# Performance work log

Measured on AMD Instinct MI355X. Metric: run time of the kernel, lower is better.

The kernel has to match this reference:

```python
import math
import jax, jax.numpy as jnp
import numpy as np

B, N, DIM = 2, 4096, 768
H, DK, DV = 8, 64, 64


def setup_inputs() -> dict:
    key = jax.random.key(0)
    ks = jax.random.split(key, 6)
    s = 0.02
    return {
        "x": jax.random.normal(ks[0], (B, N, DIM), dtype=jnp.float32),
        "Wq": jax.random.normal(ks[1], (DIM, H * DK), dtype=jnp.float32) * s,
        "Wk": jax.random.normal(ks[2], (DIM, H * DK), dtype=jnp.float32) * s,
        "Wv": jax.random.normal(ks[3], (DIM, H * DV), dtype=jnp.float32) * s,
        "Wo": jax.random.normal(ks[4], (H * DV, DIM), dtype=jnp.float32) * s,
        "bo": jax.random.normal(ks[5], (DIM,), dtype=jnp.float32) * s,
    }


def reference(x, Wq, Wk, Wv, Wo, bo):
    b, n, _ = x.shape
    # project and split heads: [B, H, N, d]
    q = (x @ Wq).reshape(b, n, H, DK).transpose(0, 2, 1, 3)
    k = (x @ Wk).reshape(b, n, H, DK).transpose(0, 2, 1, 3)
    v = (x @ Wv).reshape(b, n, H, DV).transpose(0, 2, 1, 3)
    scale = 1.0 / math.sqrt(DK)
    scores = jnp.einsum("bhnd,bhmd->bhnm", q, k) * scale  # [B,H,N,N]
    attn = jax.nn.softmax(scores, axis=-1)
    out = jnp.einsum("bhnm,bhmd->bhnd", attn, v)  # [B,H,N,DV]
    out = out.transpose(0, 2, 1, 3).reshape(b, n, H * DV)
    return out @ Wo + bo
```

## Files before the change

kernel.cpp:

```cpp
#include <hip/hip_runtime.h>
#include <hip/hip_bf16.h>

#define B_   2
#define N_   4096
#define DIM_ 768
#define H_   8
#define MROWS_ 8192

typedef __bf16 bf16x8 __attribute__((ext_vector_type(8)));
typedef __bf16 bf16x4 __attribute__((ext_vector_type(4)));
typedef float  f32x4  __attribute__((ext_vector_type(4)));

static __device__ __forceinline__ f32x4 mfma16(bf16x8 a, bf16x8 b, f32x4 c) {
    return __builtin_amdgcn_mfma_f32_16x16x32_bf16(a, b, c, 0, 0, 0);
}

#define GLDS16(g, l) \
    __builtin_amdgcn_global_load_lds((const __attribute__((address_space(1))) void*)(g), \
                                     (__attribute__((address_space(3))) void*)(l), 16, 0, 0)

__global__ void cvt_x_kernel(const float* __restrict__ x, __bf16* __restrict__ xb, int n4) {
    int i = blockIdx.x * blockDim.x + threadIdx.x;
    if (i >= n4) return;
    float4 f = reinterpret_cast<const float4*>(x)[i];
    bf16x4 o;
    o[0] = (__bf16)f.x; o[1] = (__bf16)f.y; o[2] = (__bf16)f.z; o[3] = (__bf16)f.w;
    reinterpret_cast<bf16x4*>(xb)[i] = o;
}

__global__ __launch_bounds__(256) void transpose_w_kernel(const float* __restrict__ Wq,
                                                          const float* __restrict__ Wk,
                                                          const float* __restrict__ Wv,
                                                          const float* __restrict__ Wo,
                                                          __bf16* __restrict__ wt,
                                                          __bf16* __restrict__ wot) {
    __shared__ float tile[64][65];
    const int bix = blockIdx.x;
    const float* src;
    int src_ld, rbase, cbase, dst_ld, drow, dcol;
    __bf16* dst;
    if (bix < 288) {
        int m = bix / 96, t = bix - m * 96;
        int tr = t >> 3, tc = t & 7;
        src = (m == 0) ? Wq : ((m == 1) ? Wk : Wv);
        src_ld = 512; rbase = tr * 64; cbase = tc * 64;
        dst = wt; dst_ld = 768; drow = m * 512 + tc * 64; dcol = tr * 64;
    } else {
        int t = bix - 288;
        int tr = t / 12, tc = t - tr * 12;
        src = Wo; src_ld = 768; rbase = tr * 64; cbase = tc * 64;
        dst = wot; dst_ld = 512; drow = tc * 64; dcol = tr * 64;
    }
#pragma unroll
    for (int kk = 0; kk < 4; ++kk) {
        int idx = threadIdx.x + kk * 256;
        int r = idx >> 4, c = (idx & 15) << 2;
        float4 f = *reinterpret_cast<const float4*>(&src[(size_t)(rbase + r) * src_ld + cbase + c]);
        tile[r][c] = f.x; tile[r][c + 1] = f.y; tile[r][c + 2] = f.z; tile[r][c + 3] = f.w;
    }
    __syncthreads();
#pragma unroll
    for (int kk = 0; kk < 4; ++kk) {
        int idx = threadIdx.x + kk * 256;
        int r = idx >> 4, c = (idx & 15) << 2;
        bf16x4 ov;
        ov[0] = (__bf16)tile[c][r];     ov[1] = (__bf16)tile[c + 1][r];
        ov[2] = (__bf16)tile[c + 2][r]; ov[3] = (__bf16)tile[c + 3][r];
        *reinterpret_cast<bf16x4*>(&dst[(size_t)(drow + r) * dst_ld + dcol + c]) = ov;
    }
}

template<int KSTEPS>
__device__ __forceinline__ void gemm_tile_main(const __bf16* __restrict__ A, const int lda,
                                               const int arow0,
                                               const __bf16* __restrict__ Bt, const int ldb,
                                               const int bcol0,
                                               __bf16* __restrict__ abuf,
                                               __bf16* __restrict__ bbuf,
                                               f32x4 (&acc)[4][4]) {
    const int lane = threadIdx.x & 63, wave = threadIdx.x >> 6;
    const int lr = lane & 15, lg = lane >> 4;
    const int wr = wave >> 1, wc = wave & 1;

    const int cid0 = wave * 128 + lane;
    const int cid1 = cid0 + 64;
    const __bf16* sA0 = A  + (size_t)(arow0 + (cid0 >> 2)) * lda + (cid0 & 3) * 8;
    const __bf16* sA1 = A  + (size_t)(arow0 + (cid1 >> 2)) * lda + (cid1 & 3) * 8;
    const __bf16* sB0 = Bt + (size_t)(bcol0 + (cid0 >> 2)) * ldb + (cid0 & 3) * 8;
    const __bf16* sB1 = Bt + (size_t)(bcol0 + (cid1 >> 2)) * ldb + (cid1 & 3) * 8;

    auto stage = [&](int buf, int ks) {
        __bf16* da = abuf + buf * 4096 + wave * 1024;
        __bf16* db = bbuf + buf * 4096 + wave * 1024;
        GLDS16(sA0 + ks * 32, da);
        GLDS16(sA1 + ks * 32, da + 512);
        GLDS16(sB0 + ks * 32, db);
        GLDS16(sB1 + ks * 32, db + 512);
    };

    stage(0, 0);
    asm volatile("s_waitcnt vmcnt(0)" ::: "memory");
    __syncthreads();

    const int ar_off = (wr * 64 + lr) * 32 + lg * 8;
    const int br_off = (wc * 64 + lr) * 32 + lg * 8;

    int buf = 0;
    for (int ks = 0; ks < KSTEPS; ++ks) {
        if (ks + 1 < KSTEPS) stage(buf ^ 1, ks + 1);
        const __bf16* ab = abuf + buf * 4096 + ar_off;
        const __bf16* bb = bbuf + buf * 4096 + br_off;
        bf16x8 af[4], bfr[4];
#pragma unroll
        for (int m = 0; m < 4; ++m) af[m] = *reinterpret_cast<const bf16x8*>(ab + m * 512);
#pragma unroll
        for (int n = 0; n < 4; ++n) bfr[n] = *reinterpret_cast<const bf16x8*>(bb + n * 512);
#pragma unroll
        for (int m = 0; m < 4; ++m)
#pragma unroll
            for (int n = 0; n < 4; ++n)
                acc[m][n] = mfma16(af[m], bfr[n], acc[m][n]);
        asm volatile("s_waitcnt vmcnt(0)" ::: "memory");
        __syncthreads();
        buf ^= 1;
    }
}

__global__ __launch_bounds__(256) void qkv_gemm_kernel(const __bf16* __restrict__ xb,
                                                       const __bf16* __restrict__ wt,
                                                       __bf16* __restrict__ q,
                                                       __bf16* __restrict__ k,
                                                       __bf16* __restrict__ vt) {
    __shared__ __align__(16) __bf16 abuf[2 * 4096];
    __shared__ __align__(16) __bf16 bbuf[2 * 4096];

    const int bid = blockIdx.x;
    const int vb = (bid & 7) * 96 + (bid >> 3);
    const int by = vb % 12, bx = vb / 12;

    f32x4 acc[4][4] = {};
    gemm_tile_main<24>(xb, 768, bx * 128, wt, 768, by * 128, abuf, bbuf, acc);

    const int lane = threadIdx.x & 63, wave = threadIdx.x >> 6;
    const int lr = lane & 15, lg = lane >> 4;
    const int wr = wave >> 1, wc = wave & 1;
    const int bi = (bx * 128) >> 12;
    const int nbase = (bx * 128) & 4095;

    const float QSCALE = 0.125f * 1.44269504089f;

#pragma unroll
    for (int n = 0; n < 4; ++n) {
        const int col0 = by * 128 + wc * 64 + n * 16;
        const int mtx = col0 >> 9;
        const int h   = (col0 >> 6) & 7;
        const int d0  = (col0 & 63) + lr;
        const size_t hb = (size_t)(bi * 8 + h);
#pragma unroll
        for (int m = 0; m < 4; ++m) {
            const int nn = nbase + wr * 64 + m * 16 + lg * 4;
            if (mtx == 0) {
#pragma unroll
                for (int r = 0; r < 4; ++r)
                    q[(hb * 4096 + nn + r) * 64 + d0] = (__bf16)(acc[m][n][r] * QSCALE);
            } else if (mtx == 1) {
#pragma unroll
                for (int r = 0; r < 4; ++r)
                    k[(hb * 4096 + nn + r) * 64 + d0] = (__bf16)acc[m][n][r];
            } else {
                bf16x4 ov;
#pragma unroll
                for (int r = 0; r < 4; ++r) ov[r] = (__bf16)acc[m][n][r];
                *reinterpret_cast<bf16x4*>(&vt[(hb * 64 + d0) * 4096 + nn]) = ov;
            }
        }
    }
}

__global__ __launch_bounds__(256) void attn_kernel(const __bf16* __restrict__ q,
                                                   const __bf16* __restrict__ k,
                                                   const __bf16* __restrict__ vt,
                                                   __bf16* __restrict__ o) {
    const int lane = threadIdx.x & 63, wave = threadIdx.x >> 6;
    const int lr = lane & 15, lg = lane >> 4;

    const int bid  = blockIdx.x;
    const int vbid = (bid & 7) * 64 + (bid >> 3);
    const int qtile = vbid & 31;
    const int bh    = vbid >> 5;
    const int qbase = qtile * 128 + wave * 32;

    const __bf16* Qh = q  + (size_t)bh * N_ * 64;
    const __bf16* Kh = k  + (size_t)bh * N_ * 64;
    const __bf16* Vh = vt + (size_t)bh * 64 * N_;

    __shared__ __align__(16) __bf16 kbuf[2][64][64];
    __shared__ __align__(16) __bf16 vbuf[2][64][64];

    const int l8 = lane >> 3, l7 = lane & 7;
    const int swz8 = (l7 ^ l8) * 8;

    int ksrc[4];
#pragma unroll
    for (int c = 0; c < 4; ++c) {
        int i = (wave & 1) * 32 + c * 8 + l8;
        int sig = ((i >> 4) & 1) * 32 + ((i >> 2) & 3) * 8 + ((i >> 5) & 1) * 4 + (i & 3);
        ksrc[c] = sig * 64 + swz8;
    }

    auto stage = [&](int buf, int jt) {
        const int jbase = jt * 64;
        if (wave < 2) {
            const __bf16* srcb = Kh + (size_t)jbase * 64;
            __bf16* dst = &kbuf[buf][wave * 32][0];
#pragma unroll
            for (int c = 0; c < 4; ++c)
                GLDS16(srcb + ksrc[c], dst + c * 512);
        } else {
            const int w2 = wave - 2;
            const __bf16* src = Vh + (size_t)(w2 * 32 + l8) * 4096 + jbase + swz8;
            __bf16* dst = &vbuf[buf][w2 * 32][0];
#pragma unroll
            for (int c = 0; c < 4; ++c)
                GLDS16(src + (size_t)c * 8 * 4096, dst + c * 512);
        }
    };

    bf16x8 qf[2][2];
#pragma unroll
    for (int frag = 0; frag < 2; ++frag)
#pragma unroll
        for (int kc = 0; kc < 2; ++kc)
            qf[frag][kc] = *reinterpret_cast<const bf16x8*>(
                Qh + (size_t)(qbase + frag * 16 + lr) * 64 + kc * 32 + lg * 8);

    f32x4 acc[2][4] = {};
    float lsum[2] = {0.f, 0.f};

    stage(0, 0);
    asm volatile("s_waitcnt vmcnt(0)" ::: "memory");
    __syncthreads();

    int cur = 0;
    for (int jt = 0; jt < 64; ++jt) {
        if (jt + 1 < 64) stage(cur ^ 1, jt + 1);

        const char* kb = (const char*)&kbuf[cur][0][0];
        f32x4 s[2][4] = {};
#pragma unroll
        for (int kc = 0; kc < 2; ++kc) {
#pragma unroll
            for (int cb = 0; cb < 4; ++cb) {
                const int row = cb * 16 + lr;
                bf16x8 bk = *reinterpret_cast<const bf16x8*>(
                    kb + row * 128 + (((kc * 4 + lg) ^ (lr & 7)) << 4));
                __builtin_amdgcn_s_setprio(1);
                s[0][cb] = mfma16(bk, qf[0][kc], s[0][cb]);
                s[1][cb] = mfma16(bk, qf[1][kc], s[1][cb]);
                __builtin_amdgcn_s_setprio(0);
            }
        }
        bf16x8 pk[2][2];
#pragma unroll
        for (int frag = 0; frag < 2; ++frag) {
#pragma unroll
            for (int kc = 0; kc < 2; ++kc) {
#pragma unroll
                for (int t = 0; t < 8; ++t) {
                    float p = __builtin_amdgcn_exp2f(s[frag][kc + 2 * (t >> 2)][t & 3]);
                    lsum[frag] += p;
                    pk[frag][kc][t] = (__bf16)p;
                }
            }
        }
        const char* vb = (const char*)&vbuf[cur][0][0];
#pragma unroll
        for (int kc = 0; kc < 2; ++kc) {
#pragma unroll
            for (int cbv = 0; cbv < 4; ++cbv) {
                const int row = cbv * 16 + lr;
                bf16x8 bv = *reinterpret_cast<const bf16x8*>(
                    vb + row * 128 + (((kc * 4 + lg) ^ (lr & 7)) << 4));
                __builtin_amdgcn_s_setprio(1);
                acc[0][cbv] = mfma16(pk[0][kc], bv, acc[0][cbv]);
                acc[1][cbv] = mfma16(pk[1][kc], bv, acc[1][cbv]);
                __builtin_amdgcn_s_setprio(0);
            }
        }
        asm volatile("s_waitcnt vmcnt(0)" ::: "memory");
        __syncthreads();
        cur ^= 1;
    }

    const int b = bh >> 3, h = bh & 7;
#pragma unroll
    for (int frag = 0; frag < 2; ++frag) {
        float lv = lsum[frag];
        lv += __shfl_xor(lv, 16);
        lv += __shfl_xor(lv, 32);
#pragma unroll
        for (int r = 0; r < 4; ++r) {
            float lvq = __shfl(lv, lg * 4 + r);
            float inv = 1.f / lvq;
            int row = b * N_ + qbase + frag * 16 + lg * 4 + r;
#pragma unroll
            for (int cbv = 0; cbv < 4; ++cbv)
                o[(size_t)row * 512 + h * 64 + cbv * 16 + lr] =
                    (__bf16)(acc[frag][cbv][r] * inv);
        }
    }
}

__global__ __launch_bounds__(256) void out_gemm_kernel(const __bf16* __restrict__ ob,
                                                       const __bf16* __restrict__ wot,
                                                       const float* __restrict__ bo,
                                                       float* __restrict__ out) {
    __shared__ __align__(16) __bf16 abuf[2 * 4096];
    __shared__ __align__(16) __bf16 bbuf[2 * 4096];

    const int bid = blockIdx.x;
    const int vb = (bid & 7) * 48 + (bid >> 3);
    const int by = vb % 6, bx = vb / 6;

    f32x4 acc[4][4] = {};
    gemm_tile_main<16>(ob, 512, bx * 128, wot, 512, by * 128, abuf, bbuf, acc);

    const int lane = threadIdx.x & 63, wave = threadIdx.x >> 6;
    const int lr = lane & 15, lg = lane >> 4;
    const int wr = wave >> 1, wc = wave & 1;

#pragma unroll
    for (int n = 0; n < 4; ++n) {
        const int col = by * 128 + wc * 64 + n * 16 + lr;
        const float bias = bo[col];
#pragma unroll
        for (int m = 0; m < 4; ++m) {
            const int row0 = bx * 128 + wr * 64 + m * 16 + lg * 4;
#pragma unroll
            for (int r = 0; r < 4; ++r)
                out[(size_t)(row0 + r) * 768 + col] = acc[m][n][r] + bias;
        }
    }
}

extern "C" void kernel_launch(void* const* d_in, const int* in_sizes, int n_in,
                              void* d_out, int out_size, void* d_ws, size_t ws_size,
                              hipStream_t stream) {
    const float* x  = (const float*)d_in[0];
    const float* Wq = (const float*)d_in[1];
    const float* Wk = (const float*)d_in[2];
    const float* Wv = (const float*)d_in[3];
    const float* Wo = (const float*)d_in[4];
    const float* bo = (const float*)d_in[5];
    float* out = (float*)d_out;

    char* ws = (char*)d_ws;
    __bf16* xb  = (__bf16*)(ws);
    __bf16* wt  = (__bf16*)(ws + 12582912);
    __bf16* wot = (__bf16*)(ws + 12582912 + 2359296);
    char*   p0  = ws + 12582912 + 2359296 + 786432;
    __bf16* qw  = (__bf16*)(p0);
    __bf16* kw  = (__bf16*)(p0 + 8388608);
    __bf16* vtw = (__bf16*)(p0 + 2 * (size_t)8388608);
    __bf16* obf = (__bf16*)(p0 + 3 * (size_t)8388608);

    cvt_x_kernel<<<6144, 256, 0, stream>>>(x, xb, MROWS_ * DIM_ / 4);
    transpose_w_kernel<<<384, 256, 0, stream>>>(Wq, Wk, Wv, Wo, wt, wot);
    qkv_gemm_kernel<<<768, 256, 0, stream>>>(xb, wt, qw, kw, vtw);
    attn_kernel<<<512, 256, 0, stream>>>(qw, kw, vtw, obf);
    out_gemm_kernel<<<384, 256, 0, stream>>>(obf, wot, bo, out);
}
```

Before: 141.9 us.

## Software-pipeline QK and PV across key tiles; compute row sums via MFMA

Restructures the attention inner loop into a two-stage software pipeline. The QK^T of the next key tile is issued between the exp of the current tile and its PV product, and K and V are staged separately so K runs one tile ahead. The softmax denominator is now accumulated with an MFMA against a ones vector instead of scalar adds plus cross-lane shuffles. The aim is to overlap matrix-core work with the exp (transcendental) work and remove VALU reductions, at the cost of more live registers (two score buffers). It also accumulates the denominator from bf16-rounded probabilities, which slightly changes numerics.

```diff
diff --git a/kernel.cpp b/kernel.cpp
--- a/kernel.cpp
+++ b/kernel.cpp
@@ -208,17 +208,19 @@
         ksrc[c] = sig * 64 + swz8;
     }
 
-    auto stage = [&](int buf, int jt) {
-        const int jbase = jt * 64;
+    auto stageK = [&](int buf, int jt) {
         if (wave < 2) {
-            const __bf16* srcb = Kh + (size_t)jbase * 64;
+            const __bf16* srcb = Kh + (size_t)jt * 64 * 64;
             __bf16* dst = &kbuf[buf][wave * 32][0];
 #pragma unroll
             for (int c = 0; c < 4; ++c)
                 GLDS16(srcb + ksrc[c], dst + c * 512);
-        } else {
+        }
+    };
+    auto stageV = [&](int buf, int jt) {
+        if (wave >= 2) {
             const int w2 = wave - 2;
-            const __bf16* src = Vh + (size_t)(w2 * 32 + l8) * 4096 + jbase + swz8;
+            const __bf16* src = Vh + (size_t)(w2 * 32 + l8) * 4096 + jt * 64 + swz8;
             __bf16* dst = &vbuf[buf][w2 * 32][0];
 #pragma unroll
             for (int c = 0; c < 4; ++c)
@@ -235,18 +237,14 @@
                 Qh + (size_t)(qbase + frag * 16 + lr) * 64 + kc * 32 + lg * 8);
 
     f32x4 acc[2][4] = {};
-    float lsum[2] = {0.f, 0.f};
-
-    stage(0, 0);
-    asm volatile("s_waitcnt vmcnt(0)" ::: "memory");
-    __syncthreads();
-
-    int cur = 0;
-    for (int jt = 0; jt < 64; ++jt) {
-        if (jt + 1 < 64) stage(cur ^ 1, jt + 1);
-
-        const char* kb = (const char*)&kbuf[cur][0][0];
-        f32x4 s[2][4] = {};
+    f32x4 accl[2] = {};
+    bf16x8 vones;
+#pragma unroll
+    for (int t = 0; t < 8; ++t) vones[t] = (__bf16)1.0f;
+
+    auto QK = [&](f32x4 (&s)[2][4], const __bf16* kb_) {
+        const char* kb = (const char*)kb_;
+        __builtin_amdgcn_s_setprio(1);
 #pragma unroll
         for (int kc = 0; kc < 2; ++kc) {
 #pragma unroll
@@ -254,26 +252,26 @@
                 const int row = cb * 16 + lr;
                 bf16x8 bk = *reinterpret_cast<const bf16x8*>(
                     kb + row * 128 + (((kc * 4 + lg) ^ (lr & 7)) << 4));
-                __builtin_amdgcn_s_setprio(1);
-                s[0][cb] = mfma16(bk, qf[0][kc], s[0][cb]);
-                s[1][cb] = mfma16(bk, qf[1][kc], s[1][cb]);
-                __builtin_amdgcn_s_setprio(0);
+                if (kc == 0) { s[0][cb] = mfma16(bk, qf[0][0], {}); s[1][cb] = mfma16(bk, qf[1][0], {}); }
+                else         { s[0][cb] = mfma16(bk, qf[0][1], s[0][cb]); s[1][cb] = mfma16(bk, qf[1][1], s[1][cb]); }
             }
         }
-        bf16x8 pk[2][2];
-#pragma unroll
-        for (int frag = 0; frag < 2; ++frag) {
+        __builtin_amdgcn_s_setprio(0);
+    };
+    auto EXP = [&](f32x4 (&s)[2][4], bf16x8 (&pk)[2][2]) {
+#pragma unroll
+        for (int frag = 0; frag < 2; ++frag)
 #pragma unroll
             for (int kc = 0; kc < 2; ++kc) {
 #pragma unroll
-                for (int t = 0; t < 8; ++t) {
-                    float p = __builtin_amdgcn_exp2f(s[frag][kc + 2 * (t >> 2)][t & 3]);
-                    lsum[frag] += p;
-                    pk[frag][kc][t] = (__bf16)p;
-                }
+                for (int t = 0; t < 8; ++t)
+                    pk[frag][kc][t] = (__bf16)__builtin_amdgcn_exp2f(s[frag][kc + 2 * (t >> 2)][t & 3]);
+                accl[frag] = mfma16(pk[frag][kc], vones, accl[frag]);
             }
-        }
-        const char* vb = (const char*)&vbuf[cur][0][0];
+    };
+    auto PV = [&](bf16x8 (&pk)[2][2], const __bf16* vb_) {
+        const char* vb = (const char*)vb_;
+        __builtin_amdgcn_s_setprio(1);
 #pragma unroll
         for (int kc = 0; kc < 2; ++kc) {
 #pragma unroll
@@ -281,27 +279,60 @@
                 const int row = cbv * 16 + lr;
                 bf16x8 bv = *reinterpret_cast<const bf16x8*>(
                     vb + row * 128 + (((kc * 4 + lg) ^ (lr & 7)) << 4));
-                __builtin_amdgcn_s_setprio(1);
                 acc[0][cbv] = mfma16(pk[0][kc], bv, acc[0][cbv]);
                 acc[1][cbv] = mfma16(pk[1][kc], bv, acc[1][cbv]);
-                __builtin_amdgcn_s_setprio(0);
             }
         }
+        __builtin_amdgcn_s_setprio(0);
+    };
+
+    f32x4 sA[2][4], sB[2][4];
+    bf16x8 pkA[2][2], pkB[2][2];
+
+    stageK(0, 0);
+    asm volatile("s_waitcnt vmcnt(0)" ::: "memory");
+    __syncthreads();
+
+    stageK(1, 1);
+    stageV(0, 0);
+    QK(sA, &kbuf[0][0][0]);
+    asm volatile("s_waitcnt vmcnt(0)" ::: "memory");
+    __syncthreads();
+
+    for (int t = 0; t < 31; ++t) {
+        const int jt = 2 * t + 1;
+        stageK(0, jt + 1);
+        stageV(1, jt);
+        EXP(sA, pkA);
+        QK(sB, &kbuf[1][0][0]);
+        PV(pkA, &vbuf[0][0][0]);
         asm volatile("s_waitcnt vmcnt(0)" ::: "memory");
         __syncthreads();
-        cur ^= 1;
-    }
+        stageK(1, jt + 2);
+        stageV(0, jt + 1);
+        EXP(sB, pkB);
+        QK(sA, &kbuf[0][0][0]);
+        PV(pkB, &vbuf[1][0][0]);
+        asm volatile("s_waitcnt vmcnt(0)" ::: "memory");
+        __syncthreads();
+    }
+
+    stageV(1, 63);
+    EXP(sA, pkA);
+    QK(sB, &kbuf[1][0][0]);
+    PV(pkA, &vbuf[0][0][0]);
+    asm volatile("s_waitcnt vmcnt(0)" ::: "memory");
+    __syncthreads();
+
+    EXP(sB, pkB);
+    PV(pkB, &vbuf[1][0][0]);
 
     const int b = bh >> 3, h = bh & 7;
 #pragma unroll
     for (int frag = 0; frag < 2; ++frag) {
-        float lv = lsum[frag];
-        lv += __shfl_xor(lv, 16);
-        lv += __shfl_xor(lv, 32);
 #pragma unroll
         for (int r = 0; r < 4; ++r) {
-            float lvq = __shfl(lv, lg * 4 + r);
-            float inv = 1.f / lvq;
+            float inv = 1.f / accl[frag][r];
             int row = b * N_ + qbase + frag * 16 + lg * 4 + r;
 #pragma unroll
             for (int cbv = 0; cbv < 4; ++cbv)
```

After: 125.0 us. -11.9%, faster.
